# Kernel optimization log

Hardware: AMD Instinct MI355X
Metric: run time of the kernel (lower is better)

## Reference

```python
import jax, jax.numpy as jnp
import numpy as np

NSIDE = 64
NLAT = 4 * NSIDE - 1        # 255 iso-latitude rings
NLON = 4 * NSIDE            # 256 = max pixels per ring
NPIX = 12 * NSIDE * NSIDE   # 49152 HEALPix pixels
LMAX = NLAT                 # 255
MMAX = NLON // 2 + 1        # 129
BATCH, CHAN = 8, 32


def _ring_geometry():
    # HEALPix ring scheme: ring r (0-based), 1-based i=r+1
    #  north cap i<nside: nph=4i, phi shift 0.5
    #  equatorial nside<=i<=3*nside: nph=4*nside, shift alternates {0,0.5}
    #  south cap: mirror of north cap
    nph = np.zeros(NLAT, np.int64)
    shift = np.zeros(NLAT, np.float64)
    for r in range(NLAT):
        i = r + 1
        if i < NSIDE:
            nph[r], shift[r] = 4 * i, 0.5
        elif i <= 3 * NSIDE:
            nph[r], shift[r] = 4 * NSIDE, 0.5 * ((i - NSIDE + 1) % 2)
        else:
            nph[r], shift[r] = 4 * (NLAT - r), 0.5
    offs = np.concatenate([[0], np.cumsum(nph)[:-1]])
    p = np.arange(NLON)
    mask = (p[None, :] < nph[:, None])                       # [nlat, nlon]
    idx = (offs[:, None] + p[None, :]) * mask                # padded -> 0
    phase = 2.0 * np.pi * (p[None, :] + shift[:, None]) / nph[:, None] * mask
    return idx.astype(np.int32), mask.astype(np.float32), phase.astype(np.float32)


def setup_inputs() -> dict:
    key = jax.random.key(0)
    k1, k2, k3 = jax.random.split(key, 3)
    idx, mask, phase = _ring_geometry()
    x = jax.random.normal(k1, (BATCH, CHAN, NPIX), jnp.float32)
    pct = jax.random.normal(k2, (MMAX, LMAX, NLAT), jnp.float32) * 0.1  # Legendre table stand-in
    w = jax.random.uniform(k3, (NLAT,), jnp.float32)                    # per-ring quadrature weights
    return {"x": x, "pct": pct, "w": w,
            "ring_index": jnp.asarray(idx),
            "ring_mask": jnp.asarray(mask),
            "phase": jnp.asarray(phase)}


def _healpix_rfft_real(x, ring_index, ring_mask, phase):
    # x: [..., npix] -> per-ring DFT coefficients as real pairs [..., nlat, mmax, 2]
    rings = x[..., ring_index] * ring_mask                 # [..., nlat, nlon]
    m = jnp.arange(MMAX, dtype=phase.dtype)
    ang = phase[:, :, None] * m                            # [nlat, nlon, mmax]
    fr = jnp.einsum('...kp,kpm->...km', rings, jnp.cos(ang))
    fi = -jnp.einsum('...kp,kpm->...km', rings, jnp.sin(ang))
    return jnp.stack([fr, fi], axis=-1)                    # n=2 is view_as_real axis


def reference(x, pct, w, ring_index, ring_mask, phase):
    # healpix ring rFFT, then Legendre contraction (einsum '...kmn,mlk->...lmn')
    f = _healpix_rfft_real(x, ring_index, ring_mask, phase)  # [..., nlat, mmax, 2]
    weights = pct * w                                        # [mmax, lmax, nlat]
    out = jnp.einsum('...kmn,mlk->...lmn', f, weights)       # [..., lmax, mmax, 2]
    return out
```

## Files before the change

kernel.cpp:

```cpp
#include <hip/hip_runtime.h>

#define NLAT 255
#define NLON 256
#define NPIX 49152
#define MMAX 129
#define MCS  258
#define NTBL 65
#define TROWS 264

typedef unsigned short ushort_t;
typedef __attribute__((ext_vector_type(8)))  short  bf16x8;
typedef __attribute__((ext_vector_type(4)))  short  short4v;
typedef __attribute__((ext_vector_type(16))) float  f32x16;
typedef __attribute__((ext_vector_type(4)))  float  float4v;

__device__ __forceinline__ ushort_t f2bf(float f) {
    union { float f; unsigned u; } v; v.f = f;
    unsigned r = v.u + 0x7FFFu + ((v.u >> 16) & 1u);
    return (ushort_t)(r >> 16);
}
__device__ __forceinline__ float bf2f(ushort_t h) {
    union { unsigned u; float f; } v; v.u = ((unsigned)h) << 16;
    return v.f;
}

__global__ __launch_bounds__(256) void prepK(const float* __restrict__ pct,
                                             const float* __restrict__ w,
                                             ushort_t* __restrict__ pctw) {
    const int m  = blockIdx.x;
    const int l0 = blockIdx.y * 32;
    const int t  = threadIdx.x;
    const float wk = (t < NLAT) ? w[t] : 0.f;
    for (int l = l0; l < l0 + 32; ++l) {
        float v = 0.f;
        if (l < NLAT && t < NLAT)
            v = pct[((size_t)m * NLAT + l) * NLAT + t] * wk;
        pctw[((size_t)m * 256 + l) * 256 + t] = f2bf(v);
    }
}

__global__ __launch_bounds__(256) void trigK(const float* __restrict__ phase,
                                             const float* __restrict__ mask,
                                             ushort_t* __restrict__ Ttab3) {
    const int tt  = blockIdx.x;
    const int mcs = blockIdx.y;
    const int p   = threadIdx.x;
    const int r   = (tt < 63) ? tt : (tt == 63 ? 63 : 64);
    float val = 0.f;
    if (mcs < MCS) {
        float ph = phase[r * NLON + p];
        float mk = mask[r * NLON + p];
        float fm = (float)(mcs >> 1);
        float s, c;
        __sincosf(ph * fm, &s, &c);
        val = (mcs & 1) ? (-s * mk) : (c * mk);
    }
    const int pcc = p >> 6, c = (p >> 3) & 7, j = p & 7;
    Ttab3[((((size_t)tt * 4 + pcc) * 8 + c) * TROWS + mcs) * 8 + j] = f2bf(val);
}

__global__ __launch_bounds__(256, 4) void stageA(const float* __restrict__ x,
                                                 const int* __restrict__ ring_index,
                                                 const ushort_t* __restrict__ Ttab3,
                                                 ushort_t* __restrict__ f1) {
    __shared__ __align__(16) ushort_t Rs[64 * 72];

    const int b0 = blockIdx.x * 64;
    const int r  = blockIdx.y;
    const int i1 = r + 1;
    const int nph = (i1 < 64) ? 4 * i1 : (i1 <= 192 ? 256 : 4 * (256 - i1));
    const int tbl = (i1 < 64) ? r : (i1 <= 192 ? (63 + (((i1 - 63) & 1) ^ 1)) : 254 - r);
    const int base = ring_index[r * NLON];

    const int t    = threadIdx.x;
    const int lane = t & 63;
    const int wid  = t >> 6;
    const int wrow = wid >> 1, wcol = wid & 1;
    const int lg   = lane >> 5;
    const int lc   = lane & 31;

    f32x16 acc[5];
#pragma unroll
    for (int tau = 0; tau < 5; ++tau)
#pragma unroll
        for (int q = 0; q < 16; ++q) acc[tau][q] = 0.f;

    for (int pc = 0; pc < nph; pc += 64) {
        {
            const int p0 = (t & 15) * 4;
            const bool ok = (pc + p0) < nph;
#pragma unroll
            for (int pass = 0; pass < 4; ++pass) {
                int bc = (t >> 4) + pass * 16;
                float4v v = {0.f, 0.f, 0.f, 0.f};
                if (ok) v = *(const float4v*)(x + (size_t)(b0 + bc) * NPIX + base + pc + p0);
                short4v h;
                h[0] = (short)f2bf(v[0]); h[1] = (short)f2bf(v[1]);
                h[2] = (short)f2bf(v[2]); h[3] = (short)f2bf(v[3]);
                *(short4v*)(Rs + bc * 72 + p0) = h;
            }
        }
        __syncthreads();
        const ushort_t* slab = Ttab3 + (size_t)(tbl * 4 + (pc >> 6)) * (8 * TROWS * 8);
#pragma unroll
        for (int ks = 0; ks < 4; ++ks) {
            bf16x8 a = *(const bf16x8*)(Rs + (wrow * 32 + lc) * 72 + ks * 16 + lg * 8);
            const ushort_t* bcol = slab + (size_t)(ks * 2 + lg) * (TROWS * 8);
#pragma unroll
            for (int tau = 0; tau < 5; ++tau) {
                int rr   = tau * 64 + wcol * 32 + lc;
                int trow = rr > (TROWS - 1) ? (TROWS - 1) : rr;
                bf16x8 b = *(const bf16x8*)(bcol + trow * 8);
                acc[tau] = __builtin_amdgcn_mfma_f32_32x32x16_bf16(a, b, acc[tau], 0, 0, 0);
            }
        }
        __syncthreads();
    }

    ushort_t* Olds = Rs;
#pragma unroll
    for (int tau = 0; tau < 5; ++tau) {
        __syncthreads();
        {
            const int mcsl = wcol * 32 + lc;
#pragma unroll
            for (int q = 0; q < 16; ++q) {
                int bcl = wrow * 32 + 4 * lg + (q & 3) + 8 * (q >> 2);
                Olds[mcsl * 72 + bcl] = f2bf(acc[tau][q]);
            }
        }
        __syncthreads();
        {
            int row = t >> 2;
            int mcs = tau * 64 + row;
            if (mcs < MCS) {
                int m = mcs >> 1, n = mcs & 1;
                size_t gbase = ((size_t)m * NLAT + r) * 512 + n * 256 + b0 + (t & 3) * 16;
#pragma unroll
                for (int j = 0; j < 2; ++j) {
                    bf16x8 v = *(const bf16x8*)(Olds + row * 72 + (t & 3) * 16 + j * 8);
                    *(bf16x8*)(f1 + gbase + j * 8) = v;
                }
            }
        }
    }
}

__global__ __launch_bounds__(256) void transK(const ushort_t* __restrict__ f1,
                                              ushort_t* __restrict__ f1t) {
    __shared__ __align__(16) ushort_t T[64][72];
    const int m  = blockIdx.x;
    const int k0 = blockIdx.y * 64;
    const int b0 = blockIdx.z * 64;
    const int t  = threadIdx.x;
#pragma unroll
    for (int it = 0; it < 2; ++it) {
        int id = t + it * 256;
        int kk = id >> 3, ch = id & 7;
        int k  = k0 + kk;
        bf16x8 v = {0,0,0,0,0,0,0,0};
        if (k < NLAT)
            v = *(const bf16x8*)(f1 + ((size_t)m * NLAT + k) * 512 + b0 + ch * 8);
        *(bf16x8*)(&T[kk][ch * 8]) = v;
    }
    __syncthreads();
#pragma unroll
    for (int it = 0; it < 2; ++it) {
        int id  = t + it * 256;
        int bb  = id & 63, ch8 = id >> 6;
        bf16x8 v;
#pragma unroll
        for (int j = 0; j < 8; ++j) v[j] = T[ch8 * 8 + j][bb];
        *(bf16x8*)(f1t + ((size_t)m * 512 + b0 + bb) * 256 + k0 + ch8 * 8) = v;
    }
}

__global__ __launch_bounds__(256, 2) void stageB(const ushort_t* __restrict__ f1t,
                                                 const ushort_t* __restrict__ pctw,
                                                 ushort_t* __restrict__ otmp) {
    __shared__ __align__(16) ushort_t SB[30720];
    ushort_t* As = SB;
    ushort_t* Ws = SB + 10240;
    ushort_t* Es = SB;

    const int id = blockIdx.x;
    const int m  = ((id >> 5) << 3) | (id & 7);
    if (m >= MMAX) return;
    const int sub = (id >> 3) & 3;
    const int b2t = sub * 128;

    const int t     = threadIdx.x;
    const int lane  = t & 63;
    const int wid   = t >> 6;
    const int wrow  = wid >> 1, wlcol = wid & 1;
    const int lg    = lane >> 5, lc = lane & 31;

    f32x16 acc[2][4];
#pragma unroll
    for (int i = 0; i < 2; ++i)
#pragma unroll
        for (int j = 0; j < 4; ++j)
#pragma unroll
            for (int q = 0; q < 16; ++q) acc[i][j][q] = 0.f;

    bf16x8 ra[2], rw[4];
    auto ldA = [&](int kc) {
#pragma unroll
        for (int pass = 0; pass < 2; ++pass) {
            int id2 = t + pass * 256;
            int row = id2 >> 2, ch = id2 & 3;
            ra[pass] = *(const bf16x8*)(f1t + ((size_t)m * 512 + b2t + row) * 256 + kc + ch * 8);
        }
    };
    auto ldW = [&](int kc) {
#pragma unroll
        for (int pass = 0; pass < 4; ++pass) {
            int id2 = t + pass * 256;
            int row = id2 >> 2, ch = id2 & 3;
            rw[pass] = *(const bf16x8*)(pctw + ((size_t)m * 256 + row) * 256 + kc + ch * 8);
        }
    };
    auto stA = [&](ushort_t* dst) {
#pragma unroll
        for (int pass = 0; pass < 2; ++pass) {
            int id2 = t + pass * 256;
            int row = id2 >> 2, ch = id2 & 3;
            *(bf16x8*)(dst + row * 40 + ch * 8) = ra[pass];
        }
    };
    auto stW = [&](ushort_t* dst) {
#pragma unroll
        for (int pass = 0; pass < 4; ++pass) {
            int id2 = t + pass * 256;
            int row = id2 >> 2, ch = id2 & 3;
            *(bf16x8*)(dst + row * 40 + ch * 8) = rw[pass];
        }
    };

    ldA(0); ldW(0);
    stA(As); stW(Ws);
    __syncthreads();
    int buf = 0;
    for (int kc = 0; kc < 256; kc += 32, buf ^= 1) {
        const bool more = (kc + 32) < 256;
        if (more) { ldA(kc + 32); ldW(kc + 32); }
        const ushort_t* A = As + buf * 5120;
        const ushort_t* W = Ws + buf * 10240;
#pragma unroll
        for (int ks = 0; ks < 2; ++ks) {
            const int ko = ks * 16 + lg * 8;
            bf16x8 a0 = *(const bf16x8*)(A + (wrow * 64 + lc) * 40 + ko);
            bf16x8 a1 = *(const bf16x8*)(A + (wrow * 64 + 32 + lc) * 40 + ko);
#pragma unroll
            for (int jj = 0; jj < 4; ++jj) {
                bf16x8 b = *(const bf16x8*)(W + (wlcol * 128 + jj * 32 + lc) * 40 + ko);
                acc[0][jj] = __builtin_amdgcn_mfma_f32_32x32x16_bf16(a0, b, acc[0][jj], 0, 0, 0);
                acc[1][jj] = __builtin_amdgcn_mfma_f32_32x32x16_bf16(a1, b, acc[1][jj], 0, 0, 0);
            }
        }
        if (more) { stA(As + (buf ^ 1) * 5120); stW(Ws + (buf ^ 1) * 10240); }
        __syncthreads();
    }

#pragma unroll
    for (int h = 0; h < 2; ++h) {
        if (h) __syncthreads();
        if (wlcol == h) {
#pragma unroll
            for (int i = 0; i < 2; ++i)
#pragma unroll
                for (int jj = 0; jj < 4; ++jj)
#pragma unroll
                    for (int q = 0; q < 16; ++q) {
                        int bl = wrow * 64 + i * 32 + 4 * lg + (q & 3) + 8 * (q >> 2);
                        Es[bl * 136 + jj * 32 + lc] = f2bf(acc[i][jj][q]);
                    }
        }
        __syncthreads();
#pragma unroll
        for (int it = 0; it < 8; ++it) {
            int id2 = t + it * 256;
            int row = id2 >> 4, ch = id2 & 15;
            bf16x8 v = *(const bf16x8*)(Es + row * 136 + ch * 8);
            *(bf16x8*)(otmp + (((size_t)m * 512 + b2t + row) << 8) + h * 128 + ch * 8) = v;
        }
    }
}

__global__ __launch_bounds__(256) void permuteK(const ushort_t* __restrict__ otmp,
                                                float* __restrict__ out) {
    __shared__ ushort_t L[MCS * 66];
    const int bc = blockIdx.x;
    const int l0 = blockIdx.y * 64;
    const int t  = threadIdx.x;
    const int ll = t & 63;
    const int l  = l0 + ll;
#pragma unroll 4
    for (int it = 0; it < 65; ++it) {
        int mn = (t >> 6) + it * 4;
        if (mn < MCS) {
            int mm = mn >> 1, n = mn & 1;
            ushort_t v = 0;
            if (l < NLAT)
                v = otmp[(((size_t)mm * 512 + n * 256 + bc) << 8) + l];
            L[mn * 66 + ll] = v;
        }
    }
    __syncthreads();
    for (int ll2 = 0; ll2 < 64; ++ll2) {
        int lo = l0 + ll2;
        if (lo >= NLAT) break;
        size_t rowb = ((size_t)bc * NLAT + lo) * MCS;
        out[rowb + t] = bf2f(L[t * 66 + ll2]);
        if (t < 2)
            out[rowb + 256 + t] = bf2f(L[(256 + t) * 66 + ll2]);
    }
}

extern "C" void kernel_launch(void* const* d_in, const int* in_sizes, int n_in,
                              void* d_out, int out_size, void* d_ws, size_t ws_size,
                              hipStream_t stream) {
    const float* x          = (const float*)d_in[0];
    const float* pct        = (const float*)d_in[1];
    const float* w          = (const float*)d_in[2];
    const int*   ring_index = (const int*)d_in[3];
    const float* ring_mask  = (const float*)d_in[4];
    const float* phase      = (const float*)d_in[5];
    float* out = (float*)d_out;

    char* wsb = (char*)d_ws;
    char* ob  = (char*)d_out;
    ushort_t* otmp  = (ushort_t*)wsb;
    ushort_t* f1    = (ushort_t*)(wsb + 33552384);
    ushort_t* f1t   = (ushort_t*)ob;
    ushort_t* pctw  = (ushort_t*)(ob + 33816576);
    ushort_t* Ttab3 = (ushort_t*)(ob + 50724864);

    prepK   <<<dim3(MMAX, 8),     256, 0, stream>>>(pct, w, pctw);
    trigK   <<<dim3(NTBL, TROWS), 256, 0, stream>>>(phase, ring_mask, Ttab3);
    stageA  <<<dim3(4, NLAT),     256, 0, stream>>>(x, ring_index, Ttab3, f1);
    transK  <<<dim3(MMAX, 4, 8),  256, 0, stream>>>(f1, f1t);
    stageB  <<<dim3(544),         256, 0, stream>>>(f1t, pctw, otmp);
    permuteK<<<dim3(256, 4),      256, 0, stream>>>(otmp, out);
}
```

Baseline: 137.1 us.

## Double-buffer ring chunk loads in stageA and remap block indices

Stage A now prefetches the next 64-pixel chunk of x into registers while the MFMAs run on the current chunk, using two LDS buffers so each chunk needs only one barrier. The grid becomes a flat 1D launch whose mapping groups 8 consecutive rings across the 4 batch blocks, likely to improve cache locality of the trig table and x. This costs extra registers and LDS per block, which may reduce occupancy, and launches a few blocks that exit immediately.

```diff
diff --git a/kernel.cpp b/kernel.cpp
--- a/kernel.cpp
+++ b/kernel.cpp
@@ -63,14 +63,18 @@
                                                  const int* __restrict__ ring_index,
                                                  const ushort_t* __restrict__ Ttab3,
                                                  ushort_t* __restrict__ f1) {
-    __shared__ __align__(16) ushort_t Rs[64 * 72];
-
-    const int b0 = blockIdx.x * 64;
-    const int r  = blockIdx.y;
+    __shared__ __align__(16) ushort_t Rs[2][64 * 72];
+
+    const int id = blockIdx.x;
+    const int r  = ((id >> 5) << 3) | (id & 7);
+    if (r >= NLAT) return;
+    const int b0 = ((id >> 3) & 3) * 64;
+
     const int i1 = r + 1;
     const int nph = (i1 < 64) ? 4 * i1 : (i1 <= 192 ? 256 : 4 * (256 - i1));
     const int tbl = (i1 < 64) ? r : (i1 <= 192 ? (63 + (((i1 - 63) & 1) ^ 1)) : 254 - r);
     const int base = ring_index[r * NLON];
+    const int nchunks = (nph + 63) >> 6;
 
     const int t    = threadIdx.x;
     const int lane = t & 63;
@@ -85,26 +89,42 @@
 #pragma unroll
         for (int q = 0; q < 16; ++q) acc[tau][q] = 0.f;
 
-    for (int pc = 0; pc < nph; pc += 64) {
-        {
-            const int p0 = (t & 15) * 4;
-            const bool ok = (pc + p0) < nph;
-#pragma unroll
-            for (int pass = 0; pass < 4; ++pass) {
-                int bc = (t >> 4) + pass * 16;
-                float4v v = {0.f, 0.f, 0.f, 0.f};
-                if (ok) v = *(const float4v*)(x + (size_t)(b0 + bc) * NPIX + base + pc + p0);
-                short4v h;
-                h[0] = (short)f2bf(v[0]); h[1] = (short)f2bf(v[1]);
-                h[2] = (short)f2bf(v[2]); h[3] = (short)f2bf(v[3]);
-                *(short4v*)(Rs + bc * 72 + p0) = h;
-            }
-        }
-        __syncthreads();
-        const ushort_t* slab = Ttab3 + (size_t)(tbl * 4 + (pc >> 6)) * (8 * TROWS * 8);
+    float4v rx[4];
+    const int p0 = (t & 15) * 4;
+    auto ldX = [&](int pc) {
+        const bool ok = (pc + p0) < nph;
+#pragma unroll
+        for (int pass = 0; pass < 4; ++pass) {
+            int bc = (t >> 4) + pass * 16;
+            float4v v = {0.f, 0.f, 0.f, 0.f};
+            if (ok) v = *(const float4v*)(x + (size_t)(b0 + bc) * NPIX + base + pc + p0);
+            rx[pass] = v;
+        }
+    };
+    auto stX = [&](ushort_t* dst) {
+#pragma unroll
+        for (int pass = 0; pass < 4; ++pass) {
+            int bc = (t >> 4) + pass * 16;
+            short4v h;
+            h[0] = (short)f2bf(rx[pass][0]); h[1] = (short)f2bf(rx[pass][1]);
+            h[2] = (short)f2bf(rx[pass][2]); h[3] = (short)f2bf(rx[pass][3]);
+            *(short4v*)(dst + bc * 72 + p0) = h;
+        }
+    };
+
+    ldX(0);
+    stX(Rs[0]);
+    __syncthreads();
+
+    for (int c = 0; c < nchunks; ++c) {
+        const int pc = c << 6;
+        const bool more = (c + 1) < nchunks;
+        if (more) ldX(pc + 64);
+        const ushort_t* slab = Ttab3 + (size_t)(tbl * 4 + c) * (8 * TROWS * 8);
+        const ushort_t* Rcur = Rs[c & 1];
 #pragma unroll
         for (int ks = 0; ks < 4; ++ks) {
-            bf16x8 a = *(const bf16x8*)(Rs + (wrow * 32 + lc) * 72 + ks * 16 + lg * 8);
+            bf16x8 a = *(const bf16x8*)(Rcur + (wrow * 32 + lc) * 72 + ks * 16 + lg * 8);
             const ushort_t* bcol = slab + (size_t)(ks * 2 + lg) * (TROWS * 8);
 #pragma unroll
             for (int tau = 0; tau < 5; ++tau) {
@@ -114,10 +134,11 @@
                 acc[tau] = __builtin_amdgcn_mfma_f32_32x32x16_bf16(a, b, acc[tau], 0, 0, 0);
             }
         }
-        __syncthreads();
-    }
-
-    ushort_t* Olds = Rs;
+        if (more) stX(Rs[(c + 1) & 1]);
+        __syncthreads();
+    }
+
+    ushort_t* Olds = Rs[0];
 #pragma unroll
     for (int tau = 0; tau < 5; ++tau) {
         __syncthreads();
@@ -338,7 +359,7 @@
 
     prepK   <<<dim3(MMAX, 8),     256, 0, stream>>>(pct, w, pctw);
     trigK   <<<dim3(NTBL, TROWS), 256, 0, stream>>>(phase, ring_mask, Ttab3);
-    stageA  <<<dim3(4, NLAT),     256, 0, stream>>>(x, ring_index, Ttab3, f1);
+    stageA  <<<dim3(1024),        256, 0, stream>>>(x, ring_index, Ttab3, f1);
     transK  <<<dim3(MMAX, 4, 8),  256, 0, stream>>>(f1, f1t);
     stageB  <<<dim3(544),         256, 0, stream>>>(f1t, pctw, otmp);
     permuteK<<<dim3(256, 4),      256, 0, stream>>>(otmp, out);
```

After: 143.8 us. +4.9%, slower.
